# Optimization experiments

Hardware: AMD Instinct MI355X
Metric: run time of the kernel (lower is better)

The kernel has to match this reference:

```python
import jax, jax.numpy as jnp
import numpy as np

B, S, V, D = 65536, 51, 64, 64  # batch, seq_len (= max_length), vocab (= output_dimension), output dim
E, H1, H2 = 4, 5, 7             # embedding dim and hidden widths of the tiny MLP


def setup_inputs() -> dict:
    key = jax.random.key(0)
    ks = jax.random.split(key, 8)
    x = jax.random.randint(ks[0], (B, S), 0, V, dtype=jnp.int64)
    # Per-position parameters, stacked along the leading S axis (one tiny net per position).
    emb = jax.random.normal(ks[1], (S, V, E), dtype=jnp.float32)
    W1 = jax.random.normal(ks[2], (S, H1, E), dtype=jnp.float32) * 0.5
    b1 = jnp.zeros((S, H1), dtype=jnp.float32)
    W2 = jax.random.normal(ks[3], (S, H2, H1), dtype=jnp.float32) * 0.5
    b2 = jnp.zeros((S, H2), dtype=jnp.float32)
    W3 = jax.random.normal(ks[4], (S, D, H2), dtype=jnp.float32) * 0.5
    b3 = jnp.zeros((S, D), dtype=jnp.float32)
    return {"x": x, "emb": emb, "W1": W1, "b1": b1, "W2": W2, "b2": b2, "W3": W3, "b3": b3}


def reference(x, emb, W1, b1, W2, b2, W3, b3):
    S_ = emb.shape[0]
    pos = jnp.arange(S_)[None, :]                       # [1, S]
    e = emb[pos, x]                                     # [B, S, E] per-position embedding lookup
    h1 = jax.nn.leaky_relu(jnp.einsum('bse,she->bsh', e, W1) + b1)   # [B, S, H1]
    h2 = jax.nn.leaky_relu(jnp.einsum('bsh,sgh->bsg', h1, W2) + b2)  # [B, S, H2]
    y = jnp.tanh(jnp.einsum('bsg,sdg->bsd', h2, W3) + b3)            # [B, S, D]
    return jnp.sum(y, axis=1)                           # [B, D] sum over positions
```

## Files before the change

### kernel.cpp

```cpp
#include <hip/hip_runtime.h>
#include <hip/hip_fp16.h>

constexpr int S  = 51;
constexpr int V  = 64;
constexpr int E  = 4;
constexpr int H1 = 5;
constexpr int H2 = 7;
constexpr int D  = 64;

__global__ void build_table_kernel(const float* __restrict__ emb,
                                   const float* __restrict__ W1,
                                   const float* __restrict__ b1,
                                   const float* __restrict__ W2,
                                   const float* __restrict__ b2,
                                   const float* __restrict__ W3,
                                   const float* __restrict__ b3,
                                   __half* __restrict__ Y) {
  const int sv = blockIdx.x;
  const int s  = sv >> 6;
  const int d  = threadIdx.x;

  float e[E];
#pragma unroll
  for (int i = 0; i < E; ++i) e[i] = emb[sv * E + i];

  float h1[H1];
#pragma unroll
  for (int h = 0; h < H1; ++h) {
    float a = b1[s * H1 + h];
#pragma unroll
    for (int i = 0; i < E; ++i) a = fmaf(W1[(s * H1 + h) * E + i], e[i], a);
    h1[h] = (a >= 0.f) ? a : 0.01f * a;
  }

  float h2[H2];
#pragma unroll
  for (int g = 0; g < H2; ++g) {
    float a = b2[s * H2 + g];
#pragma unroll
    for (int h = 0; h < H1; ++h) a = fmaf(W2[(s * H2 + g) * H1 + h], h1[h], a);
    h2[g] = (a >= 0.f) ? a : 0.01f * a;
  }

  float a = b3[s * D + d];
#pragma unroll
  for (int g = 0; g < H2; ++g) a = fmaf(W3[(s * D + d) * H2 + g], h2[g], a);

  Y[sv * D + d] = __float2half(tanhf(a));
}

__global__ __launch_bounds__(256) void gather_sum_kernel(
    const int* __restrict__ x, const __half* __restrict__ Y,
    float* __restrict__ out, int B) {
  const int lane  = threadIdx.x & 63;
  const int li    = lane & 7;
  const int wid   = threadIdx.x >> 6;
  const int row   = (blockIdx.x * 4 + wid) * 8 + (lane >> 3);

  int tok[7];
#pragma unroll
  for (int j = 0; j < 7; ++j) {
    const int s = j * 8 + li;
    tok[j] = (s < S) ? (x[row * S + s] + (s << 6)) : 0;
  }

  const int rgsel = lane & 56;
  const int li16  = li << 4;
  const char* Yb  = (const char*)Y;

  float acc[8];
#pragma unroll
  for (int k = 0; k < 8; ++k) acc[k] = 0.f;

#pragma unroll
  for (int c = 0; c < 13; ++c) {
    __half2 a16[4];
#pragma unroll
    for (int k = 0; k < 4; ++k) a16[k] = __half2(__float2half(0.f), __float2half(0.f));

#pragma unroll
    for (int j = 0; j < 4; ++j) {
      const int s = c * 4 + j;
      if (s < S) {
        const int r = __shfl(tok[s >> 3], rgsel | (s & 7), 64);
        const uint4 v = *reinterpret_cast<const uint4*>(Yb + ((r << 7) | li16));
        union { uint4 u; __half2 h[4]; } cv; cv.u = v;
#pragma unroll
        for (int k = 0; k < 4; ++k) a16[k] = __hadd2(a16[k], cv.h[k]);
      }
    }

#pragma unroll
    for (int k = 0; k < 4; ++k) {
      const float2 f = __half22float2(a16[k]);
      acc[2 * k]     += f.x;
      acc[2 * k + 1] += f.y;
    }
  }

  float4* o = reinterpret_cast<float4*>(out + row * D + (li << 3));
  o[0] = make_float4(acc[0], acc[1], acc[2], acc[3]);
  o[1] = make_float4(acc[4], acc[5], acc[6], acc[7]);
}

extern "C" void kernel_launch(void* const* d_in, const int* in_sizes, int n_in,
                              void* d_out, int out_size, void* d_ws, size_t ws_size,
                              hipStream_t stream) {
  const int*   x   = (const int*)d_in[0];
  const float* emb = (const float*)d_in[1];
  const float* W1  = (const float*)d_in[2];
  const float* b1  = (const float*)d_in[3];
  const float* W2  = (const float*)d_in[4];
  const float* b2  = (const float*)d_in[5];
  const float* W3  = (const float*)d_in[6];
  const float* b3  = (const float*)d_in[7];

  const int B = in_sizes[0] / S;
  __half* Y = (__half*)d_ws;

  build_table_kernel<<<S * V, D, 0, stream>>>(emb, W1, b1, W2, b2, W3, b3, Y);

  gather_sum_kernel<<<B / 32, 256, 0, stream>>>(x, Y, (float*)d_out, B);
}
```

Measured before the change: 97.83 us.

## Stage lookup table chunks in LDS and process 256 rows per block

The gather kernel now copies 13-position slices of the fp16 lookup table into shared memory and stages each block's token indices in LDS. Each thread then accumulates 8 rows from LDS instead of issuing scattered global/L2 gathers. This is meant to cut L2 gather traffic, at the cost of very large LDS use, one block per CU, barriers between chunk loads, and possible LDS bank conflicts.

Result: slower. 127.0 us (+29.8%).

```diff
diff --git a/kernel.cpp b/kernel.cpp
--- a/kernel.cpp
+++ b/kernel.cpp
@@ -7,6 +7,9 @@
 constexpr int H1 = 5;
 constexpr int H2 = 7;
 constexpr int D  = 64;
+
+constexpr int ROWS  = 256;
+constexpr int MAXSC = 13;
 
 __global__ void build_table_kernel(const float* __restrict__ emb,
                                    const float* __restrict__ W1,
@@ -49,58 +52,80 @@
   Y[sv * D + d] = __float2half(tanhf(a));
 }
 
-__global__ __launch_bounds__(256) void gather_sum_kernel(
+__global__ __launch_bounds__(256, 1) void gather_sum_kernel(
     const int* __restrict__ x, const __half* __restrict__ Y,
-    float* __restrict__ out, int B) {
-  const int lane  = threadIdx.x & 63;
-  const int li    = lane & 7;
-  const int wid   = threadIdx.x >> 6;
-  const int row   = (blockIdx.x * 4 + wid) * 8 + (lane >> 3);
+    float* __restrict__ out) {
+  __shared__ __align__(16) __half tab[MAXSC * V * D];
+  __shared__ __align__(16) int    tok[ROWS * S];
 
-  int tok[7];
+  const int tid     = threadIdx.x;
+  const int rowbase = blockIdx.x * ROWS;
+
+  for (int i = tid; i < ROWS * S; i += 256) tok[i] = x[rowbase * S + i] << 7;
+
+  const int li   = tid & 7;
+  const int rix  = (tid >> 3) & 31;
+  const int li16 = li << 4;
+
+  float acc[8][8];
 #pragma unroll
-  for (int j = 0; j < 7; ++j) {
-    const int s = j * 8 + li;
-    tok[j] = (s < S) ? (x[row * S + s] + (s << 6)) : 0;
-  }
+  for (int a = 0; a < 8; ++a)
+#pragma unroll
+    for (int b = 0; b < 8; ++b) acc[a][b] = 0.f;
 
-  const int rgsel = lane & 56;
-  const int li16  = li << 4;
-  const char* Yb  = (const char*)Y;
+  __half2 a16[8][4];
+#pragma unroll
+  for (int a = 0; a < 8; ++a)
+#pragma unroll
+    for (int k = 0; k < 4; ++k) a16[a][k] = __half2(__float2half(0.f), __float2half(0.f));
 
-  float acc[8];
+  const char* tabb = (const char*)tab;
+
+  for (int c = 0; c < 4; ++c) {
+    const int s0 = c * 13;
+    const int sc = (c < 3) ? 13 : 12;
+
+    __syncthreads();
+    {
+      const uint4* src = (const uint4*)(Y + s0 * (V * D));
+      uint4*       dst = (uint4*)tab;
+      const int n4 = sc * (V * D / 8);
+      for (int i = tid; i < n4; i += 256) dst[i] = src[i];
+    }
+    __syncthreads();
+
+    for (int sl = 0; sl < sc; ++sl) {
+      const int tokoff = rix * S + s0 + sl;
+      const int slbase = sl * (V * D * 2) + li16;
 #pragma unroll
-  for (int k = 0; k < 8; ++k) acc[k] = 0.f;
-
-#pragma unroll
-  for (int c = 0; c < 13; ++c) {
-    __half2 a16[4];
-#pragma unroll
-    for (int k = 0; k < 4; ++k) a16[k] = __half2(__float2half(0.f), __float2half(0.f));
-
-#pragma unroll
-    for (int j = 0; j < 4; ++j) {
-      const int s = c * 4 + j;
-      if (s < S) {
-        const int r = __shfl(tok[s >> 3], rgsel | (s & 7), 64);
-        const uint4 v = *reinterpret_cast<const uint4*>(Yb + ((r << 7) | li16));
+      for (int ri = 0; ri < 8; ++ri) {
+        const int taddr = tok[ri * 32 * S + tokoff];
+        const uint4 v = *(const uint4*)(tabb + (slbase + taddr));
         union { uint4 u; __half2 h[4]; } cv; cv.u = v;
 #pragma unroll
-        for (int k = 0; k < 4; ++k) a16[k] = __hadd2(a16[k], cv.h[k]);
+        for (int k = 0; k < 4; ++k) a16[ri][k] = __hadd2(a16[ri][k], cv.h[k]);
       }
-    }
-
+      if ((sl & 3) == 3 || sl == sc - 1) {
 #pragma unroll
-    for (int k = 0; k < 4; ++k) {
-      const float2 f = __half22float2(a16[k]);
-      acc[2 * k]     += f.x;
-      acc[2 * k + 1] += f.y;
+        for (int ri = 0; ri < 8; ++ri)
+#pragma unroll
+          for (int k = 0; k < 4; ++k) {
+            const float2 f = __half22float2(a16[ri][k]);
+            acc[ri][2 * k]     += f.x;
+            acc[ri][2 * k + 1] += f.y;
+            a16[ri][k] = __half2(__float2half(0.f), __float2half(0.f));
+          }
+      }
     }
   }
 
-  float4* o = reinterpret_cast<float4*>(out + row * D + (li << 3));
-  o[0] = make_float4(acc[0], acc[1], acc[2], acc[3]);
-  o[1] = make_float4(acc[4], acc[5], acc[6], acc[7]);
+#pragma unroll
+  for (int ri = 0; ri < 8; ++ri) {
+    const int row = rowbase + ri * 32 + rix;
+    float4* o = (float4*)(out + row * D + li * 8);
+    o[0] = make_float4(acc[ri][0], acc[ri][1], acc[ri][2], acc[ri][3]);
+    o[1] = make_float4(acc[ri][4], acc[ri][5], acc[ri][6], acc[ri][7]);
+  }
 }
 
 extern "C" void kernel_launch(void* const* d_in, const int* in_sizes, int n_in,
@@ -120,5 +145,5 @@
 
   build_table_kernel<<<S * V, D, 0, stream>>>(emb, W1, b1, W2, b2, W3, b3, Y);
 
-  gather_sum_kernel<<<B / 32, 256, 0, stream>>>(x, Y, (float*)d_out, B);
+  gather_sum_kernel<<<B / ROWS, 256, 0, stream>>>(x, Y, (float*)d_out);
 }
```

## Stage lookup table chunks in double-buffered LDS for gather-sum

Applied to the files above, without the earlier changes.

The gather kernel now uses 1024-thread blocks of 128 rows each. It copies the per-position fp16 table into shared memory in chunks of 4 positions (32 KB per buffer) with double buffering: the next chunk is loaded into registers while the current chunk is gathered. Random gathers then hit LDS instead of global/L2. The cost is a block-wide barrier per chunk, 64 KB of LDS per block, and every block re-reading the full 400 KB table, which limits occupancy.

Result: slower. 237.5 us (+142.8%).

```diff
diff --git a/kernel.cpp b/kernel.cpp
--- a/kernel.cpp
+++ b/kernel.cpp
@@ -7,6 +7,9 @@
 constexpr int H1 = 5;
 constexpr int H2 = 7;
 constexpr int D  = 64;
+
+constexpr int CH = 4;
+constexpr int NC = 13;
 
 __global__ void build_table_kernel(const float* __restrict__ emb,
                                    const float* __restrict__ W1,
@@ -49,56 +52,86 @@
   Y[sv * D + d] = __float2half(tanhf(a));
 }
 
-__global__ __launch_bounds__(256) void gather_sum_kernel(
+__global__ __launch_bounds__(1024, 8) void gather_sum_kernel(
     const int* __restrict__ x, const __half* __restrict__ Y,
-    float* __restrict__ out, int B) {
-  const int lane  = threadIdx.x & 63;
+    float* __restrict__ out) {
+  __shared__ __align__(16) __half buf[2][CH * V * D];
+
+  const int tid   = threadIdx.x;
+  const int lane  = tid & 63;
   const int li    = lane & 7;
-  const int wid   = threadIdx.x >> 6;
-  const int row   = (blockIdx.x * 4 + wid) * 8 + (lane >> 3);
+  const int wid   = tid >> 6;
+  const int row   = blockIdx.x * 128 + wid * 8 + (lane >> 3);
 
   int tok[7];
 #pragma unroll
   for (int j = 0; j < 7; ++j) {
     const int s = j * 8 + li;
-    tok[j] = (s < S) ? (x[row * S + s] + (s << 6)) : 0;
+    tok[j] = (s < S) ? (x[row * S + s] << 7) : 0;
   }
 
   const int rgsel = lane & 56;
   const int li16  = li << 4;
-  const char* Yb  = (const char*)Y;
+  const char* bufb = (const char*)buf;
 
   float acc[8];
 #pragma unroll
   for (int k = 0; k < 8; ++k) acc[k] = 0.f;
 
+  {
+    const uint4* src = (const uint4*)Y;
+    uint4* dst = (uint4*)buf[0];
+    dst[tid * 2]     = src[tid * 2];
+    dst[tid * 2 + 1] = src[tid * 2 + 1];
+  }
+
 #pragma unroll
-  for (int c = 0; c < 13; ++c) {
+  for (int c = 0; c < NC; ++c) {
+    __syncthreads();
+
+    uint4 v0, v1;
+    bool do_stage = false;
+    int g0 = 0, g1 = 0;
+    if (c + 1 < NC) {
+      const int n16 = ((c + 1 < NC - 1) ? CH : 3) * 512;
+      const uint4* src = (const uint4*)(Y + (c + 1) * CH * (V * D));
+      g0 = tid * 2; g1 = tid * 2 + 1;
+      do_stage = true;
+      v0 = (g0 < n16) ? src[g0] : uint4{0, 0, 0, 0};
+      v1 = (g1 < n16) ? src[g1] : uint4{0, 0, 0, 0};
+    }
+
     __half2 a16[4];
 #pragma unroll
     for (int k = 0; k < 4; ++k) a16[k] = __half2(__float2half(0.f), __float2half(0.f));
 
+    const char* base = bufb + ((c & 1) << 15);
 #pragma unroll
-    for (int j = 0; j < 4; ++j) {
-      const int s = c * 4 + j;
+    for (int j = 0; j < CH; ++j) {
+      const int s = c * CH + j;
       if (s < S) {
-        const int r = __shfl(tok[s >> 3], rgsel | (s & 7), 64);
-        const uint4 v = *reinterpret_cast<const uint4*>(Yb + ((r << 7) | li16));
+        const int t = __shfl(tok[s >> 3], rgsel | (s & 7), 64);
+        const uint4 v = *(const uint4*)(base + ((j << 13) + t + li16));
         union { uint4 u; __half2 h[4]; } cv; cv.u = v;
 #pragma unroll
         for (int k = 0; k < 4; ++k) a16[k] = __hadd2(a16[k], cv.h[k]);
       }
     }
-
 #pragma unroll
     for (int k = 0; k < 4; ++k) {
       const float2 f = __half22float2(a16[k]);
       acc[2 * k]     += f.x;
       acc[2 * k + 1] += f.y;
     }
+
+    if (do_stage) {
+      uint4* dst = (uint4*)buf[(c + 1) & 1];
+      dst[g0] = v0;
+      dst[g1] = v1;
+    }
   }
 
-  float4* o = reinterpret_cast<float4*>(out + row * D + (li << 3));
+  float4* o = (float4*)(out + row * D + li * 8);
   o[0] = make_float4(acc[0], acc[1], acc[2], acc[3]);
   o[1] = make_float4(acc[4], acc[5], acc[6], acc[7]);
 }
@@ -120,5 +153,5 @@
 
   build_table_kernel<<<S * V, D, 0, stream>>>(emb, W1, b1, W2, b2, W3, b3, Y);
 
-  gather_sum_kernel<<<B / 32, 256, 0, stream>>>(x, Y, (float*)d_out, B);
+  gather_sum_kernel<<<B / 128, 1024, 0, stream>>>(x, Y, (float*)d_out);
 }
```

## Stream lookup table through LDS with double-buffered direct global-to-LDS loads

Applied to the files above, without the earlier changes.

The gather kernel now stages three positions of the fp16 lookup table at a time (24 KB chunks) into shared memory using global_load_lds, double-buffered across 17 chunks. Token indices for 128 rows per block are preloaded into LDS. Each 1024-thread block then gathers its rows from LDS instead of doing random global/L2 reads. The aim is to replace scattered cache traffic with fast LDS reads, at the cost of copying the whole 418 KB table once per block, 17 block-wide barriers per block, and heavier LDS use that limits how many blocks fit per CU.

After: 160.7 us. +64.3%, slower.

```diff
diff --git a/kernel.cpp b/kernel.cpp
--- a/kernel.cpp
+++ b/kernel.cpp
@@ -7,6 +7,11 @@
 constexpr int H1 = 5;
 constexpr int H2 = 7;
 constexpr int D  = 64;
+
+constexpr int CH   = 3;
+constexpr int NC   = 17;
+constexpr int RPB  = 128;
+constexpr int TPAD = 52;
 
 __global__ void build_table_kernel(const float* __restrict__ emb,
                                    const float* __restrict__ W1,
@@ -49,45 +54,73 @@
   Y[sv * D + d] = __float2half(tanhf(a));
 }
 
-__global__ __launch_bounds__(256) void gather_sum_kernel(
+__device__ __forceinline__ void gload_lds16(const void* g, void* l) {
+  __builtin_amdgcn_global_load_lds(
+      (const __attribute__((address_space(1))) unsigned int*)g,
+      (__attribute__((address_space(3))) unsigned int*)l, 16, 0, 0);
+}
+
+__global__ __launch_bounds__(1024, 4) void gather_sum_kernel(
     const int* __restrict__ x, const __half* __restrict__ Y,
-    float* __restrict__ out, int B) {
-  const int lane  = threadIdx.x & 63;
-  const int li    = lane & 7;
-  const int wid   = threadIdx.x >> 6;
-  const int row   = (blockIdx.x * 4 + wid) * 8 + (lane >> 3);
+    float* __restrict__ out) {
+  __shared__ __align__(16) __half buf[2][CH * V * D];
+  __shared__ int tokl[RPB * TPAD];
 
-  int tok[7];
-#pragma unroll
-  for (int j = 0; j < 7; ++j) {
-    const int s = j * 8 + li;
-    tok[j] = (s < S) ? (x[row * S + s] + (s << 6)) : 0;
+  const int tid  = threadIdx.x;
+  const int lane = tid & 63;
+  const int li   = lane & 7;
+  const int rg   = lane >> 3;
+  const int wid  = tid >> 6;
+  const int rowbase = blockIdx.x * RPB;
+
+  for (int i = tid; i < RPB * S; i += 1024) {
+    const int r = i / S;
+    const int s = i - r * S;
+    tokl[r * TPAD + s] = x[rowbase * S + i] << 7;
   }
 
-  const int rgsel = lane & 56;
-  const int li16  = li << 4;
-  const char* Yb  = (const char*)Y;
+  const char* bufb = (const char*)buf;
+  const char* Yb   = (const char*)Y;
+  const int   li16 = li << 4;
+  const int   trow = ((wid << 3) | rg) * TPAD;
+
+  {
+    const char* src = Yb;
+    char* dst = (char*)buf[0];
+    gload_lds16(src + wid * 1024 + lane * 16, dst + wid * 1024);
+    if (wid < 8)
+      gload_lds16(src + (wid + 16) * 1024 + lane * 16, dst + (wid + 16) * 1024);
+  }
 
   float acc[8];
 #pragma unroll
   for (int k = 0; k < 8; ++k) acc[k] = 0.f;
 
-#pragma unroll
-  for (int c = 0; c < 13; ++c) {
+  for (int c = 0; c < NC; ++c) {
+    __syncthreads();
+
+    if (c + 1 < NC) {
+      const char* src = Yb + (c + 1) * (CH * V * D * 2);
+      char* dst = (char*)buf[(c + 1) & 1];
+      gload_lds16(src + wid * 1024 + lane * 16, dst + wid * 1024);
+      if (wid < 8)
+        gload_lds16(src + (wid + 16) * 1024 + lane * 16, dst + (wid + 16) * 1024);
+    }
+
+    const char* base = bufb + ((c & 1) ? (CH * V * D * 2) : 0);
+    const int sbase = c * CH;
+
     __half2 a16[4];
 #pragma unroll
     for (int k = 0; k < 4; ++k) a16[k] = __half2(__float2half(0.f), __float2half(0.f));
 
 #pragma unroll
-    for (int j = 0; j < 4; ++j) {
-      const int s = c * 4 + j;
-      if (s < S) {
-        const int r = __shfl(tok[s >> 3], rgsel | (s & 7), 64);
-        const uint4 v = *reinterpret_cast<const uint4*>(Yb + ((r << 7) | li16));
-        union { uint4 u; __half2 h[4]; } cv; cv.u = v;
+    for (int j = 0; j < CH; ++j) {
+      const int toff = tokl[trow + sbase + j];
+      const uint4 v = *(const uint4*)(base + ((j << 13) + toff + li16));
+      union { uint4 u; __half2 h[4]; } cv; cv.u = v;
 #pragma unroll
-        for (int k = 0; k < 4; ++k) a16[k] = __hadd2(a16[k], cv.h[k]);
-      }
+      for (int k = 0; k < 4; ++k) a16[k] = __hadd2(a16[k], cv.h[k]);
     }
 
 #pragma unroll
@@ -98,7 +131,8 @@
     }
   }
 
-  float4* o = reinterpret_cast<float4*>(out + row * D + (li << 3));
+  const int row = rowbase + (wid << 3) + rg;
+  float4* o = (float4*)(out + row * D + li * 8);
   o[0] = make_float4(acc[0], acc[1], acc[2], acc[3]);
   o[1] = make_float4(acc[4], acc[5], acc[6], acc[7]);
 }
@@ -120,5 +154,5 @@
 
   build_table_kernel<<<S * V, D, 0, stream>>>(emb, W1, b1, W2, b2, W3, b3, Y);
 
-  gather_sum_kernel<<<B / 32, 256, 0, stream>>>(x, Y, (float*)d_out, B);
+  gather_sum_kernel<<<B / RPB, 1024, 0, stream>>>(x, Y, (float*)d_out);
 }
```
